# Optimization experiments

Measured on AMD Instinct MI355X. Metric: run time of the kernel, lower is better.

## Reference

```python
import jax, jax.numpy as jnp
import numpy as np

N = 50000        # nodes
E = 800000       # edges (avg degree 16)
IN = 128         # in_feats
HF = 128         # h_feats
HID = (IN + HF) // 2  # 128, per math.floor((h_feats+in_feats)/2)


def setup_inputs() -> dict:
    key = jax.random.key(0)
    ks = jax.random.split(key, 13)

    def glorot(k, fan_in, fan_out):
        s = (2.0 / (fan_in + fan_out)) ** 0.5
        return jax.random.normal(k, (fan_in, fan_out), jnp.float32) * s

    dims = [(IN, HID), (HID, HID), (HID, HID), (HID, HID), (HID, HF)]
    inp = {
        "in_feat": jax.random.normal(ks[0], (N, IN), jnp.float32),
        "src": jax.random.randint(ks[1], (E,), 0, N),
        "dst": jax.random.randint(ks[2], (E,), 0, N),
    }
    for i, (a, b) in enumerate(dims):
        inp[f"W{i+1}"] = glorot(ks[3 + i], a, b)
        inp[f"b{i+1}"] = jnp.zeros((b,), jnp.float32)
    return inp


def reference(in_feat, src, dst, W1, W2, W3, W4, W5, b1, b2, b3, b4, b5):
    # DGL GraphConv, norm='both': y = D_in^{-1/2} * A^T * (D_out^{-1/2} * x) @ W + b
    ones = jnp.ones((src.shape[0],), in_feat.dtype)
    deg_out = jnp.clip(jax.ops.segment_sum(ones, src, num_segments=N), 1.0)
    deg_in = jnp.clip(jax.ops.segment_sum(ones, dst, num_segments=N), 1.0)
    ns = (deg_out ** -0.5)[:, None]  # source-side norm [N,1]
    nd = (deg_in ** -0.5)[:, None]   # dest-side norm   [N,1]

    def conv(x, W, b):
        m = jax.ops.segment_sum((x * ns)[src], dst, num_segments=N)  # [N,D]
        return (m * nd) @ W + b

    h = in_feat
    for W, b in ((W1, b1), (W2, b2), (W3, b3), (W4, b4), (W5, b5)):
        h = jax.nn.relu(conv(h, W, b))

    # vectorized version of the per-element Python double loop threshold
    h_clone = jnp.where(h >= 0.5, jnp.float32(1.0), jnp.float32(0.0))
    return h, h_clone
```

## Files before the change

### kernel.cpp

```cpp
#include <hip/hip_runtime.h>

#define FEAT 128
#define RANGE 12800
#define NSLICE 64

typedef _Float16 half8 __attribute__((ext_vector_type(8)));
typedef _Float16 half4v __attribute__((ext_vector_type(4)));
typedef float f32x4 __attribute__((ext_vector_type(4)));

__global__ __launch_bounds__(1024) void hist_kernel(const int* __restrict__ src,
                                                    const int* __restrict__ dst,
                                                    unsigned* __restrict__ partialD,
                                                    unsigned* __restrict__ partialS,
                                                    int E, int NP) {
    __shared__ unsigned hpk[RANGE / 2];
    int per = (NP / RANGE) * NSLICE;
    int b = blockIdx.x;
    int halfsel = b / per;
    int q = b % per;
    int r = q / NSLICE;
    int s = q % NSLICE;
    const int* arr = halfsel ? src : dst;
    unsigned* out = halfsel ? partialS : partialD;
    int v0 = r * RANGE;
    int tid = threadIdx.x;
    for (int i = tid; i < RANGE / 2; i += 1024) hpk[i] = 0;
    __syncthreads();
    int e0 = (int)((long long)E * s / NSLICE);
    int e1 = (int)((long long)E * (s + 1) / NSLICE);
    for (int e = e0 + tid; e < e1; e += 1024) {
        unsigned d = (unsigned)(arr[e] - v0);
        if (d < RANGE) atomicAdd(&hpk[d >> 1], (d & 1) ? 65536u : 1u);
    }
    __syncthreads();
    size_t wbase = ((size_t)s * NP + v0) >> 1;
    for (int i = tid; i < RANGE / 2; i += 1024) out[wbase + i] = hpk[i];
}

__global__ __launch_bounds__(256) void prep1_kernel(const unsigned short* __restrict__ pD,
                                                    const unsigned short* __restrict__ pS,
                                                    int* __restrict__ blockSums,
                                                    float* __restrict__ ns,
                                                    float* __restrict__ nd,
                                                    const float* __restrict__ Wa,
                                                    const float* __restrict__ Wb,
                                                    const float* __restrict__ Wc,
                                                    const float* __restrict__ Wd,
                                                    const float* __restrict__ We,
                                                    _Float16* __restrict__ w16t,
                                                    _Float16* __restrict__ wrt,
                                                    int NP, int n, int sb) {
    int tid = threadIdx.x;
    int b = blockIdx.x;
    if (b < sb) {
        __shared__ int buf[256];
        int v = b * 256 + tid;
        int ssum = 0, osum = 0;
        #pragma unroll
        for (int s = 0; s < NSLICE; ++s) {
            ssum += pD[(size_t)s * NP + v];
            osum += pS[(size_t)s * NP + v];
        }
        if (v < n) {
            ns[v] = 1.0f / sqrtf((float)(osum < 1 ? 1 : osum));
            nd[v] = 1.0f / sqrtf((float)(ssum < 1 ? 1 : ssum));
        }
        buf[tid] = ssum;
        __syncthreads();
        #pragma unroll
        for (int off = 1; off < 256; off <<= 1) {
            int t = (tid >= off) ? buf[tid - off] : 0;
            __syncthreads();
            buf[tid] += t;
            __syncthreads();
        }
        if (tid == 255) blockSums[b] = buf[255];
    } else {
        int gid = (b - sb) * 256 + tid;
        int l = gid >> 14;
        int idx = gid & 16383;
        int col = idx >> 7;
        int k = idx & 127;
        const float* Wp = (l == 0) ? Wa : (l == 1) ? Wb : (l == 2) ? Wc : (l == 3) ? Wd : We;
        float w = Wp[k * FEAT + col];
        _Float16 h = (_Float16)w;
        _Float16 r = (_Float16)(w - (float)h);
        w16t[gid] = h;
        wrt[gid] = r;
    }
}

__global__ __launch_bounds__(256) void prep2_kernel(const unsigned short* __restrict__ pD,
                                                    const int* __restrict__ blockSums,
                                                    int* __restrict__ cursorV,
                                                    int* __restrict__ offsc,
                                                    int NP, int n, int nb) {
    __shared__ int buf[256];
    int tid = threadIdx.x;
    int b = blockIdx.x;
    int bsv = (tid < nb) ? blockSums[tid] : 0;
    buf[tid] = bsv;
    __syncthreads();
    #pragma unroll
    for (int off = 1; off < 256; off <<= 1) {
        int t = (tid >= off) ? buf[tid - off] : 0;
        __syncthreads();
        buf[tid] += t;
        __syncthreads();
    }
    int myoff = (b > 0) ? buf[b - 1] : 0;
    __syncthreads();
    int v = b * 256 + tid;
    int ssum = 0;
    #pragma unroll
    for (int s = 0; s < NSLICE; ++s) ssum += pD[(size_t)s * NP + v];
    buf[tid] = ssum;
    __syncthreads();
    #pragma unroll
    for (int off = 1; off < 256; off <<= 1) {
        int t = (tid >= off) ? buf[tid - off] : 0;
        __syncthreads();
        buf[tid] += t;
        __syncthreads();
    }
    int o = myoff + buf[tid] - ssum;
    if (v <= n) offsc[v] = o;
    int* cv = cursorV + (size_t)v * NSLICE;
    #pragma unroll
    for (int s = 0; s < NSLICE; ++s) {
        int val = pD[(size_t)s * NP + v];
        cv[s] = o;
        o += val;
    }
}

__global__ __launch_bounds__(1024) void fill_kernel(const int* __restrict__ src,
                                                    const int* __restrict__ dst,
                                                    const int* __restrict__ cursorV,
                                                    int* __restrict__ esrc, int E, int NP) {
    __shared__ int cur[RANGE];
    int b = blockIdx.x;
    int r = b / NSLICE;
    int inner = b % NSLICE;
    int s = ((inner & 7) << 3) | (inner >> 3);
    int v0 = r * RANGE;
    int tid = threadIdx.x;
    for (int i = tid; i < RANGE; i += 1024)
        cur[i] = cursorV[(size_t)(v0 + i) * NSLICE + s];
    __syncthreads();
    int e0 = (int)((long long)E * s / NSLICE);
    int e1 = (int)((long long)E * (s + 1) / NSLICE);
    for (int e = e0 + tid; e < e1; e += 1024) {
        unsigned dd = (unsigned)(dst[e] - v0);
        if (dd < RANGE) {
            int p = atomicAdd(&cur[dd], 1);
            esrc[p] = src[e];
        }
    }
}

__global__ void prescale_kernel(const float* __restrict__ x, const float* __restrict__ ns,
                                _Float16* __restrict__ xh, int n) {
    int i = blockIdx.x * blockDim.x + threadIdx.x;
    if (i >= n * (FEAT / 8)) return;
    int v = i >> 4;
    float w = ns[v];
    float4 t0 = ((const float4*)x)[i * 2];
    float4 t1 = ((const float4*)x)[i * 2 + 1];
    half8 h;
    h[0] = (_Float16)(t0.x * w); h[1] = (_Float16)(t0.y * w);
    h[2] = (_Float16)(t0.z * w); h[3] = (_Float16)(t0.w * w);
    h[4] = (_Float16)(t1.x * w); h[5] = (_Float16)(t1.y * w);
    h[6] = (_Float16)(t1.z * w); h[7] = (_Float16)(t1.w * w);
    ((float4*)xh)[i] = __builtin_bit_cast(float4, h);
}

__global__ __launch_bounds__(256) void agg_kernel(const _Float16* __restrict__ x,
                                                  const int* __restrict__ offs,
                                                  const int* __restrict__ esrc,
                                                  const float* __restrict__ nd,
                                                  float* __restrict__ m, int n) {
    int gid = blockIdx.x * blockDim.x + threadIdx.x;
    int v = gid >> 6;
    if (v >= n) return;
    int lane = threadIdx.x & 63;
    int q = lane >> 4;
    int c = lane & 15;
    int s0 = offs[v], s1 = offs[v + 1];
    float a0[8] = {0,0,0,0,0,0,0,0};
    float a1[8] = {0,0,0,0,0,0,0,0};
    float a2[8] = {0,0,0,0,0,0,0,0};
    float a3[8] = {0,0,0,0,0,0,0,0};
    int j = s0 + q;
    for (; j + 12 < s1; j += 16) {
        int e0 = esrc[j], e1 = esrc[j + 4], e2 = esrc[j + 8], e3 = esrc[j + 12];
        float4 r0 = ((const float4*)(x + (size_t)e0 * FEAT))[c];
        float4 r1 = ((const float4*)(x + (size_t)e1 * FEAT))[c];
        float4 r2 = ((const float4*)(x + (size_t)e2 * FEAT))[c];
        float4 r3 = ((const float4*)(x + (size_t)e3 * FEAT))[c];
        half8 h0 = __builtin_bit_cast(half8, r0);
        half8 h1 = __builtin_bit_cast(half8, r1);
        half8 h2 = __builtin_bit_cast(half8, r2);
        half8 h3 = __builtin_bit_cast(half8, r3);
        #pragma unroll
        for (int k = 0; k < 8; ++k) {
            a0[k] += (float)h0[k];
            a1[k] += (float)h1[k];
            a2[k] += (float)h2[k];
            a3[k] += (float)h3[k];
        }
    }
    for (; j < s1; j += 4) {
        int e0 = esrc[j];
        float4 r0 = ((const float4*)(x + (size_t)e0 * FEAT))[c];
        half8 h0 = __builtin_bit_cast(half8, r0);
        #pragma unroll
        for (int k = 0; k < 8; ++k) a0[k] += (float)h0[k];
    }
    float r[8];
    #pragma unroll
    for (int k = 0; k < 8; ++k) r[k] = (a0[k] + a1[k]) + (a2[k] + a3[k]);
    #pragma unroll
    for (int k = 0; k < 8; ++k) {
        r[k] += __shfl_xor(r[k], 16);
        r[k] += __shfl_xor(r[k], 32);
    }
    if (lane < 16) {
        float sc = nd[v];
        float4 o0, o1;
        o0.x = r[0] * sc; o0.y = r[1] * sc; o0.z = r[2] * sc; o0.w = r[3] * sc;
        o1.x = r[4] * sc; o1.y = r[5] * sc; o1.z = r[6] * sc; o1.w = r[7] * sc;
        ((float4*)(m + (size_t)v * FEAT))[c * 2] = o0;
        ((float4*)(m + (size_t)v * FEAT))[c * 2 + 1] = o1;
    }
}

template<int MODE>
__global__ __launch_bounds__(256) void gemm_kernel(const float* __restrict__ M,
                                                   const _Float16* __restrict__ w16t,
                                                   const _Float16* __restrict__ wrt,
                                                   const float* __restrict__ bias,
                                                   const float* __restrict__ nsv,
                                                   _Float16* __restrict__ outh,
                                                   float* __restrict__ outf,
                                                   float* __restrict__ out2, int n) {
    __shared__ _Float16 sh[40960];
    _Float16* A16s = sh;
    _Float16* Ars  = sh + 4096;
    _Float16* W16s = sh + 8192;
    _Float16* Wrs  = sh + 24576;
    int tid = threadIdx.x;
    int r0 = blockIdx.x * 32;

    #pragma unroll
    for (int j = 0; j < 8; ++j) {
        int i = tid + j * 256;
        int col = i >> 4, ch = i & 15;
        int d = col * 16 + (ch ^ (col & 7));
        ((float4*)W16s)[d] = ((const float4*)w16t)[i];
        ((float4*)Wrs)[d]  = ((const float4*)wrt)[i];
    }
    #pragma unroll
    for (int j = 0; j < 4; ++j) {
        int i = tid + j * 256;
        int row = i >> 5, c4 = i & 31;
        int gr = r0 + row;
        float4 v = make_float4(0.f, 0.f, 0.f, 0.f);
        if (gr < n) v = ((const float4*)(M + (size_t)gr * FEAT))[c4];
        half4v h, rr;
        h[0] = (_Float16)v.x; h[1] = (_Float16)v.y; h[2] = (_Float16)v.z; h[3] = (_Float16)v.w;
        rr[0] = (_Float16)(v.x - (float)h[0]); rr[1] = (_Float16)(v.y - (float)h[1]);
        rr[2] = (_Float16)(v.z - (float)h[2]); rr[3] = (_Float16)(v.w - (float)h[3]);
        int d = row * 128 + (((c4 >> 1) ^ (row & 7)) << 3) + ((c4 & 1) << 2);
        *(half4v*)(A16s + d) = h;
        *(half4v*)(Ars + d) = rr;
    }
    __syncthreads();

    int lane = tid & 63;
    int w = tid >> 6;
    int l15 = lane & 15;
    int q = lane >> 4;
    int rbase = (w & 1) * 16 + l15;
    int cbase = (w >> 1) * 64;

    f32x4 acc[4] = {{0.f,0.f,0.f,0.f},{0.f,0.f,0.f,0.f},{0.f,0.f,0.f,0.f},{0.f,0.f,0.f,0.f}};
    #pragma unroll
    for (int ks = 0; ks < 4; ++ks) {
        int chunk = ks * 4 + q;
        int aoff = rbase * 128 + ((chunk ^ (rbase & 7)) << 3);
        half8 a16 = *(const half8*)(A16s + aoff);
        half8 ar  = *(const half8*)(Ars + aoff);
        #pragma unroll
        for (int ct = 0; ct < 4; ++ct) {
            int col = cbase + ct * 16 + l15;
            int boff = col * 128 + ((chunk ^ (col & 7)) << 3);
            half8 b16 = *(const half8*)(W16s + boff);
            half8 br  = *(const half8*)(Wrs + boff);
            acc[ct] = __builtin_amdgcn_mfma_f32_16x16x32_f16(a16, b16, acc[ct], 0, 0, 0);
            acc[ct] = __builtin_amdgcn_mfma_f32_16x16x32_f16(a16, br,  acc[ct], 0, 0, 0);
            acc[ct] = __builtin_amdgcn_mfma_f32_16x16x32_f16(ar,  b16, acc[ct], 0, 0, 0);
        }
    }

    int rloc = (w & 1) * 16 + q * 4;
    __syncthreads();
    if (MODE == 0) {
        _Float16* hstage = sh;
        float scv[4];
        #pragma unroll
        for (int reg = 0; reg < 4; ++reg) {
            int row = r0 + rloc + reg;
            scv[reg] = (row < n) ? nsv[row] : 1.0f;
        }
        #pragma unroll
        for (int ct = 0; ct < 4; ++ct) {
            int col = cbase + ct * 16 + l15;
            float b = bias[col];
            #pragma unroll
            for (int reg = 0; reg < 4; ++reg) {
                float h = acc[ct][reg] + b;
                h = h > 0.f ? h : 0.f;
                hstage[(rloc + reg) * 128 + col] = (_Float16)(h * scv[reg]);
            }
        }
        __syncthreads();
        #pragma unroll
        for (int j = 0; j < 2; ++j) {
            int i = tid + j * 256;
            int row = i >> 4, c16 = i & 15;
            if (r0 + row < n)
                ((float4*)(outh + (size_t)(r0 + row) * FEAT))[c16] =
                    ((const float4*)hstage)[i];
        }
    } else {
        float* fstage = (float*)sh;
        #pragma unroll
        for (int ct = 0; ct < 4; ++ct) {
            int col = cbase + ct * 16 + l15;
            float b = bias[col];
            #pragma unroll
            for (int reg = 0; reg < 4; ++reg) {
                float h = acc[ct][reg] + b;
                h = h > 0.f ? h : 0.f;
                fstage[(rloc + reg) * 128 + col] = h;
            }
        }
        __syncthreads();
        #pragma unroll
        for (int j = 0; j < 4; ++j) {
            int i = tid + j * 256;
            int row = i >> 5, c8 = i & 31;
            if (r0 + row < n) {
                float4 hv = ((const float4*)fstage)[i];
                ((float4*)(outf + (size_t)(r0 + row) * FEAT))[c8] = hv;
                float4 cv;
                cv.x = hv.x >= 0.5f ? 1.f : 0.f; cv.y = hv.y >= 0.5f ? 1.f : 0.f;
                cv.z = hv.z >= 0.5f ? 1.f : 0.f; cv.w = hv.w >= 0.5f ? 1.f : 0.f;
                ((float4*)(out2 + (size_t)(r0 + row) * FEAT))[c8] = cv;
            }
        }
    }
}

extern "C" void kernel_launch(void* const* d_in, const int* in_sizes, int n_in,
                              void* d_out, int out_size, void* d_ws, size_t ws_size,
                              hipStream_t stream) {
    const float* in_feat = (const float*)d_in[0];
    const int*   src     = (const int*)d_in[1];
    const int*   dst     = (const int*)d_in[2];
    const float* W[5] = {(const float*)d_in[3], (const float*)d_in[5], (const float*)d_in[7],
                         (const float*)d_in[9], (const float*)d_in[11]};
    const float* B[5] = {(const float*)d_in[4], (const float*)d_in[6], (const float*)d_in[8],
                         (const float*)d_in[10], (const float*)d_in[12]};
    const int E = in_sizes[1];
    const int N = in_sizes[0] / FEAT;
    const int NRANGE = (N + RANGE - 1) / RANGE;
    const int NP = NRANGE * RANGE;
    const size_t MTOT = (size_t)NP * NSLICE;

    char* ws = (char*)d_ws;
    size_t off = 0;
    auto alloc = [&](size_t bytes) { size_t o = off; off += (bytes + 255) & ~size_t(255); return o; };
    unsigned* partialD = (unsigned*)(ws + alloc(MTOT * 2));
    size_t    pS_off   = alloc(MTOT * 2);
    unsigned* partialS = (unsigned*)(ws + pS_off);
    int*      esrc     = (int*)(ws + pS_off);
    size_t    cV_off   = alloc(MTOT * 4);
    int*      cursorV  = (int*)(ws + cV_off);
    _Float16* xh       = (_Float16*)(ws + cV_off);
    float*    ns       = (float*)(ws + alloc((size_t)N * 4));
    float*    nd       = (float*)(ws + alloc((size_t)N * 4));
    int*      offsc    = (int*)(ws + alloc((size_t)(N + 1) * 4));
    int*      blockSums = (int*)(ws + alloc(1024));
    _Float16* w16t     = (_Float16*)(ws + alloc(5 * 16384 * 2));
    _Float16* wrt      = (_Float16*)(ws + alloc(5 * 16384 * 2));

    float* out_h = (float*)d_out;
    float* out_c = out_h + (size_t)N * FEAT;

    const int histBlocks = 2 * NRANGE * NSLICE;
    const int scanBlocks = NP / 256;

    hist_kernel<<<histBlocks, 1024, 0, stream>>>(src, dst, partialD, partialS, E, NP);
    prep1_kernel<<<scanBlocks + 320, 256, 0, stream>>>((const unsigned short*)partialD,
                                                       (const unsigned short*)partialS,
                                                       blockSums, ns, nd,
                                                       W[0], W[1], W[2], W[3], W[4],
                                                       w16t, wrt, NP, N, scanBlocks);
    prep2_kernel<<<scanBlocks, 256, 0, stream>>>((const unsigned short*)partialD, blockSums,
                                                 cursorV, offsc, NP, N, scanBlocks);
    fill_kernel<<<NRANGE * NSLICE, 1024, 0, stream>>>(src, dst, cursorV, esrc, E, NP);
    prescale_kernel<<<(N * (FEAT / 8) + 255) / 256, 256, 0, stream>>>(in_feat, ns, xh, N);

    const int agg_blocks = (int)(((size_t)N * 64 + 255) / 256);
    const int gemm_blocks = (N + 31) / 32;

    for (int l = 0; l < 5; ++l) {
        agg_kernel<<<agg_blocks, 256, 0, stream>>>(xh, offsc, esrc, nd, out_h, N);
        if (l < 4)
            gemm_kernel<0><<<gemm_blocks, 256, 0, stream>>>(out_h, w16t + (size_t)l * 16384,
                                                            wrt + (size_t)l * 16384, B[l], ns,
                                                            xh, nullptr, nullptr, N);
        else
            gemm_kernel<1><<<gemm_blocks, 256, 0, stream>>>(out_h, w16t + (size_t)l * 16384,
                                                            wrt + (size_t)l * 16384, B[l], nullptr,
                                                            nullptr, out_h, out_c, N);
    }
}
```

Baseline: 433.8 us.

## Hardcode node range, transpose cursor layout, fuse prescale into prep2

The histogram now covers all nodes in one block per slice, using dynamic LDS sized for a fixed 51200-node padded range, so each edge is no longer scanned once per range. The cursor array is stored slice-major so the fill kernel can load its cursors with contiguous vector reads, and fill now works over larger 25600-node ranges. The prescale kernel is folded into prep2 as extra blocks, and xh gets its own buffer instead of aliasing the cursor array, which removes one launch. The hardcoded NPC means the code only handles N up to 51200 and needs large dynamic LDS allocations.

```diff
diff --git a/kernel.cpp b/kernel.cpp
--- a/kernel.cpp
+++ b/kernel.cpp
@@ -1,8 +1,9 @@
 #include <hip/hip_runtime.h>
 
 #define FEAT 128
-#define RANGE 12800
 #define NSLICE 64
+#define NPC 51200
+#define RANGE_F 25600
 
 typedef _Float16 half8 __attribute__((ext_vector_type(8)));
 typedef _Float16 half4v __attribute__((ext_vector_type(4)));
@@ -12,29 +13,25 @@
                                                     const int* __restrict__ dst,
                                                     unsigned* __restrict__ partialD,
                                                     unsigned* __restrict__ partialS,
-                                                    int E, int NP) {
-    __shared__ unsigned hpk[RANGE / 2];
-    int per = (NP / RANGE) * NSLICE;
+                                                    int E) {
+    extern __shared__ unsigned hpk[];
     int b = blockIdx.x;
-    int halfsel = b / per;
-    int q = b % per;
-    int r = q / NSLICE;
-    int s = q % NSLICE;
+    int halfsel = b >> 6;
+    int s = b & 63;
     const int* arr = halfsel ? src : dst;
     unsigned* out = halfsel ? partialS : partialD;
-    int v0 = r * RANGE;
     int tid = threadIdx.x;
-    for (int i = tid; i < RANGE / 2; i += 1024) hpk[i] = 0;
+    for (int i = tid; i < NPC / 2; i += 1024) hpk[i] = 0;
     __syncthreads();
     int e0 = (int)((long long)E * s / NSLICE);
     int e1 = (int)((long long)E * (s + 1) / NSLICE);
     for (int e = e0 + tid; e < e1; e += 1024) {
-        unsigned d = (unsigned)(arr[e] - v0);
-        if (d < RANGE) atomicAdd(&hpk[d >> 1], (d & 1) ? 65536u : 1u);
+        unsigned d = (unsigned)arr[e];
+        atomicAdd(&hpk[d >> 1], (d & 1) ? 65536u : 1u);
     }
     __syncthreads();
-    size_t wbase = ((size_t)s * NP + v0) >> 1;
-    for (int i = tid; i < RANGE / 2; i += 1024) out[wbase + i] = hpk[i];
+    size_t wbase = ((size_t)s * NPC) >> 1;
+    for (int i = tid; i < NPC / 2; i += 1024) out[wbase + i] = hpk[i];
 }
 
 __global__ __launch_bounds__(256) void prep1_kernel(const unsigned short* __restrict__ pD,
@@ -49,7 +46,7 @@
                                                     const float* __restrict__ We,
                                                     _Float16* __restrict__ w16t,
                                                     _Float16* __restrict__ wrt,
-                                                    int NP, int n, int sb) {
+                                                    int n, int sb) {
     int tid = threadIdx.x;
     int b = blockIdx.x;
     if (b < sb) {
@@ -58,8 +55,8 @@
         int ssum = 0, osum = 0;
         #pragma unroll
         for (int s = 0; s < NSLICE; ++s) {
-            ssum += pD[(size_t)s * NP + v];
-            osum += pS[(size_t)s * NP + v];
+            ssum += pD[(size_t)s * NPC + v];
+            osum += pS[(size_t)s * NPC + v];
         }
         if (v < n) {
             ns[v] = 1.0f / sqrtf((float)(osum < 1 ? 1 : osum));
@@ -92,87 +89,90 @@
 
 __global__ __launch_bounds__(256) void prep2_kernel(const unsigned short* __restrict__ pD,
                                                     const int* __restrict__ blockSums,
-                                                    int* __restrict__ cursorV,
+                                                    int* __restrict__ cursorVT,
                                                     int* __restrict__ offsc,
-                                                    int NP, int n, int nb) {
-    __shared__ int buf[256];
+                                                    const float* __restrict__ xf,
+                                                    const float* __restrict__ ns,
+                                                    _Float16* __restrict__ xh,
+                                                    int n, int nb) {
     int tid = threadIdx.x;
     int b = blockIdx.x;
-    int bsv = (tid < nb) ? blockSums[tid] : 0;
-    buf[tid] = bsv;
-    __syncthreads();
-    #pragma unroll
-    for (int off = 1; off < 256; off <<= 1) {
-        int t = (tid >= off) ? buf[tid - off] : 0;
-        __syncthreads();
-        buf[tid] += t;
-        __syncthreads();
-    }
-    int myoff = (b > 0) ? buf[b - 1] : 0;
-    __syncthreads();
-    int v = b * 256 + tid;
-    int ssum = 0;
-    #pragma unroll
-    for (int s = 0; s < NSLICE; ++s) ssum += pD[(size_t)s * NP + v];
-    buf[tid] = ssum;
-    __syncthreads();
-    #pragma unroll
-    for (int off = 1; off < 256; off <<= 1) {
-        int t = (tid >= off) ? buf[tid - off] : 0;
-        __syncthreads();
-        buf[tid] += t;
-        __syncthreads();
-    }
-    int o = myoff + buf[tid] - ssum;
-    if (v <= n) offsc[v] = o;
-    int* cv = cursorV + (size_t)v * NSLICE;
-    #pragma unroll
-    for (int s = 0; s < NSLICE; ++s) {
-        int val = pD[(size_t)s * NP + v];
-        cv[s] = o;
-        o += val;
+    if (b < nb) {
+        __shared__ int buf[256];
+        int bsv = (tid < nb) ? blockSums[tid] : 0;
+        buf[tid] = bsv;
+        __syncthreads();
+        #pragma unroll
+        for (int off = 1; off < 256; off <<= 1) {
+            int t = (tid >= off) ? buf[tid - off] : 0;
+            __syncthreads();
+            buf[tid] += t;
+            __syncthreads();
+        }
+        int myoff = (b > 0) ? buf[b - 1] : 0;
+        __syncthreads();
+        int v = b * 256 + tid;
+        int ssum = 0;
+        #pragma unroll
+        for (int s = 0; s < NSLICE; ++s) ssum += pD[(size_t)s * NPC + v];
+        buf[tid] = ssum;
+        __syncthreads();
+        #pragma unroll
+        for (int off = 1; off < 256; off <<= 1) {
+            int t = (tid >= off) ? buf[tid - off] : 0;
+            __syncthreads();
+            buf[tid] += t;
+            __syncthreads();
+        }
+        int o = myoff + buf[tid] - ssum;
+        if (v <= n) offsc[v] = o;
+        #pragma unroll
+        for (int s = 0; s < NSLICE; ++s) {
+            int val = pD[(size_t)s * NPC + v];
+            cursorVT[(size_t)s * NPC + v] = o;
+            o += val;
+        }
+    } else {
+        int i = (b - nb) * 256 + tid;
+        if (i < n * (FEAT / 8)) {
+            int v = i >> 4;
+            float w = ns[v];
+            float4 t0 = ((const float4*)xf)[i * 2];
+            float4 t1 = ((const float4*)xf)[i * 2 + 1];
+            half8 h;
+            h[0] = (_Float16)(t0.x * w); h[1] = (_Float16)(t0.y * w);
+            h[2] = (_Float16)(t0.z * w); h[3] = (_Float16)(t0.w * w);
+            h[4] = (_Float16)(t1.x * w); h[5] = (_Float16)(t1.y * w);
+            h[6] = (_Float16)(t1.z * w); h[7] = (_Float16)(t1.w * w);
+            ((float4*)xh)[i] = __builtin_bit_cast(float4, h);
+        }
     }
 }
 
 __global__ __launch_bounds__(1024) void fill_kernel(const int* __restrict__ src,
                                                     const int* __restrict__ dst,
-                                                    const int* __restrict__ cursorV,
-                                                    int* __restrict__ esrc, int E, int NP) {
-    __shared__ int cur[RANGE];
+                                                    const int* __restrict__ cursorVT,
+                                                    int* __restrict__ esrc, int E) {
+    extern __shared__ int cur[];
     int b = blockIdx.x;
     int r = b / NSLICE;
     int inner = b % NSLICE;
     int s = ((inner & 7) << 3) | (inner >> 3);
-    int v0 = r * RANGE;
+    int v0 = r * RANGE_F;
     int tid = threadIdx.x;
-    for (int i = tid; i < RANGE; i += 1024)
-        cur[i] = cursorV[(size_t)(v0 + i) * NSLICE + s];
+    const int4* csrc = (const int4*)(cursorVT + (size_t)s * NPC + v0);
+    for (int i = tid; i < RANGE_F / 4; i += 1024)
+        ((int4*)cur)[i] = csrc[i];
     __syncthreads();
     int e0 = (int)((long long)E * s / NSLICE);
     int e1 = (int)((long long)E * (s + 1) / NSLICE);
     for (int e = e0 + tid; e < e1; e += 1024) {
         unsigned dd = (unsigned)(dst[e] - v0);
-        if (dd < RANGE) {
+        if (dd < RANGE_F) {
             int p = atomicAdd(&cur[dd], 1);
             esrc[p] = src[e];
         }
     }
-}
-
-__global__ void prescale_kernel(const float* __restrict__ x, const float* __restrict__ ns,
-                                _Float16* __restrict__ xh, int n) {
-    int i = blockIdx.x * blockDim.x + threadIdx.x;
-    if (i >= n * (FEAT / 8)) return;
-    int v = i >> 4;
-    float w = ns[v];
-    float4 t0 = ((const float4*)x)[i * 2];
-    float4 t1 = ((const float4*)x)[i * 2 + 1];
-    half8 h;
-    h[0] = (_Float16)(t0.x * w); h[1] = (_Float16)(t0.y * w);
-    h[2] = (_Float16)(t0.z * w); h[3] = (_Float16)(t0.w * w);
-    h[4] = (_Float16)(t1.x * w); h[5] = (_Float16)(t1.y * w);
-    h[6] = (_Float16)(t1.z * w); h[7] = (_Float16)(t1.w * w);
-    ((float4*)xh)[i] = __builtin_bit_cast(float4, h);
 }
 
 __global__ __launch_bounds__(256) void agg_kernel(const _Float16* __restrict__ x,
@@ -375,9 +375,7 @@
                          (const float*)d_in[10], (const float*)d_in[12]};
     const int E = in_sizes[1];
     const int N = in_sizes[0] / FEAT;
-    const int NRANGE = (N + RANGE - 1) / RANGE;
-    const int NP = NRANGE * RANGE;
-    const size_t MTOT = (size_t)NP * NSLICE;
+    const size_t MTOT = (size_t)NPC * NSLICE;
 
     char* ws = (char*)d_ws;
     size_t off = 0;
@@ -386,9 +384,8 @@
     size_t    pS_off   = alloc(MTOT * 2);
     unsigned* partialS = (unsigned*)(ws + pS_off);
     int*      esrc     = (int*)(ws + pS_off);
-    size_t    cV_off   = alloc(MTOT * 4);
-    int*      cursorV  = (int*)(ws + cV_off);
-    _Float16* xh       = (_Float16*)(ws + cV_off);
+    int*      cursorVT = (int*)(ws + alloc(MTOT * 4));
+    _Float16* xh       = (_Float16*)(ws + alloc((size_t)N * FEAT * 2));
     float*    ns       = (float*)(ws + alloc((size_t)N * 4));
     float*    nd       = (float*)(ws + alloc((size_t)N * 4));
     int*      offsc    = (int*)(ws + alloc((size_t)(N + 1) * 4));
@@ -399,19 +396,20 @@
     float* out_h = (float*)d_out;
     float* out_c = out_h + (size_t)N * FEAT;
 
-    const int histBlocks = 2 * NRANGE * NSLICE;
-    const int scanBlocks = NP / 256;
-
-    hist_kernel<<<histBlocks, 1024, 0, stream>>>(src, dst, partialD, partialS, E, NP);
+    const int scanBlocks = NPC / 256;
+    const int psBlocks = (N * (FEAT / 8) + 255) / 256;
+
+    hist_kernel<<<2 * NSLICE, 1024, (NPC / 2) * 4, stream>>>(src, dst, partialD, partialS, E);
     prep1_kernel<<<scanBlocks + 320, 256, 0, stream>>>((const unsigned short*)partialD,
                                                        (const unsigned short*)partialS,
                                                        blockSums, ns, nd,
                                                        W[0], W[1], W[2], W[3], W[4],
-                                                       w16t, wrt, NP, N, scanBlocks);
-    prep2_kernel<<<scanBlocks, 256, 0, stream>>>((const unsigned short*)partialD, blockSums,
-                                                 cursorV, offsc, NP, N, scanBlocks);
-    fill_kernel<<<NRANGE * NSLICE, 1024, 0, stream>>>(src, dst, cursorV, esrc, E, NP);
-    prescale_kernel<<<(N * (FEAT / 8) + 255) / 256, 256, 0, stream>>>(in_feat, ns, xh, N);
+                                                       w16t, wrt, N, scanBlocks);
+    prep2_kernel<<<scanBlocks + psBlocks, 256, 0, stream>>>((const unsigned short*)partialD,
+                                                            blockSums, cursorVT, offsc,
+                                                            in_feat, ns, xh, N, scanBlocks);
+    fill_kernel<<<(NPC / RANGE_F) * NSLICE, 1024, RANGE_F * 4, stream>>>(src, dst, cursorVT,
+                                                                         esrc, E);
 
     const int agg_blocks = (int)(((size_t)N * 64 + 255) / 256);
     const int gemm_blocks = (N + 31) / 32;
```

After: 416.8 us. 3.9% less time.
